# Optimization experiments

Hardware: AMD Instinct MI355X
Metric: run time of the kernel (lower is better)

Reference implementation:

```python
import jax, jax.numpy as jnp
import numpy as np


def _unit(v):
    return v / jnp.linalg.norm(v, axis=-1, keepdims=True)


def setup_inputs() -> dict:
    key = jax.random.key(0)
    k1, k2, k3, k4 = jax.random.split(key, 4)
    N, M = 20000, 6890
    scan_vertices = jax.random.normal(k1, (1, N, 3), dtype=jnp.float32)
    template_vertices = jax.random.normal(k2, (1, M, 3), dtype=jnp.float32)
    # normals are unit vectors in practice
    scan_normals = _unit(jax.random.normal(k3, (N, 3), dtype=jnp.float32))
    template_normals = _unit(jax.random.normal(k4, (M, 3), dtype=jnp.float32))
    return {
        "scan_vertices": scan_vertices,
        "template_vertices": template_vertices,
        "scan_normals": scan_normals,
        "template_normals": template_normals,
        "K_knn": 15,
    }


def reference(scan_vertices, template_vertices, scan_normals, template_normals, K_knn):
    sv = scan_vertices.reshape(-1, 3)       # [N,3]
    tv = template_vertices.reshape(-1, 3)   # [M,3]
    # Brute-force pairwise distances [M,N] (vectorizes the per-vertex loop)
    dist = jnp.linalg.norm(sv[None, :, :] - tv[:, None, :], axis=-1)
    # NOTE: torch.topk defaults to largest=True, so the original selects the
    # K LARGEST distances. lax.top_k also returns the largest -> faithful.
    _, knn_idx = jax.lax.top_k(dist, K_knn)                 # [M,K]
    knn_normals = scan_normals[knn_idx]                     # [M,K,3]
    dot = jnp.sum(knn_normals * template_normals[:, None, :], axis=-1)  # [M,K]
    angle_deg = jnp.degrees(jnp.arccos(jnp.clip(dot, -1.0, 1.0)))
    best = jnp.argmin(angle_deg, axis=1)                    # [M]
    sel = jnp.take_along_axis(knn_idx, best[:, None], axis=1)[:, 0]  # [M]
    mse = jnp.mean(jnp.linalg.norm(sv[sel] - tv, axis=1))
    return mse
```

## Files before the change

kernel.cpp:

```cpp
#include <hip/hip_runtime.h>
#include <math.h>


constexpr int K = 15;
constexpr int NBUCK = 256;
constexpr int WAVES = 4;

__device__ __forceinline__ int bucket_of(float k2) {
    int b = (int)(k2 * 8.0f);
    b = b > (NBUCK - 1) ? (NBUCK - 1) : b;
    return (NBUCK - 1) - b;
}

__global__ __launch_bounds__(256) void scatter_kernel(
    const float* __restrict__ sv,
    float4*      __restrict__ sorted,
    float*       __restrict__ smax,
    int N, int nb)
{
    __shared__ int h[NBUCK];
    __shared__ int startSh[NBUCK];
    __shared__ int cursor[NBUCK];
    const int t    = threadIdx.x;
    const int base = blockIdx.x * 256;

    h[t] = 0;
    __syncthreads();

#pragma unroll 4
    for (int i = t; i < base; i += 256) {
        float x = sv[3*i], y = sv[3*i+1], z = sv[3*i+2];
        atomicAdd(&h[bucket_of(fmaf(x, x, fmaf(y, y, z*z)))], 1);
    }
    __syncthreads();
    const int mine = h[t];
    __syncthreads();

    float px = 0.0f, py = 0.0f, pz = 0.0f, pk2 = 0.0f;
    const bool has = (base + t) < N;
    if (has) {
        px  = sv[3*(base+t)]; py = sv[3*(base+t)+1]; pz = sv[3*(base+t)+2];
        pk2 = fmaf(px, px, fmaf(py, py, pz*pz));
        atomicAdd(&h[bucket_of(pk2)], 1);
    }
#pragma unroll 4
    for (int i = base + 256 + t; i < N; i += 256) {
        float x = sv[3*i], y = sv[3*i+1], z = sv[3*i+2];
        atomicAdd(&h[bucket_of(fmaf(x, x, fmaf(y, y, z*z)))], 1);
    }
    __syncthreads();
    const int total = h[t];

    for (int d = 1; d < NBUCK; d <<= 1) {
        int u = (t >= d) ? h[t - d] : 0;
        __syncthreads();
        h[t] += u;
        __syncthreads();
    }
    const int startv = h[t] - total;
    startSh[t] = startv;
    cursor[t]  = startv + mine;
    __syncthreads();

    if (blockIdx.x == 0) {
        for (int j = t; j < nb; j += 256) {
            int pos = j * 64;
            int lo = 0, hi = NBUCK - 1;
            while (lo < hi) {
                int mid = (lo + hi + 1) >> 1;
                if (startSh[mid] <= pos) lo = mid; else hi = mid - 1;
            }
            int bOrig = (NBUCK - 1) - lo;
            smax[j] = sqrtf((float)(bOrig + 1) * 0.125f);
        }
    }

    if (has) {
        int pos = atomicAdd(&cursor[bucket_of(pk2)], 1);
        sorted[pos] = make_float4(px, py, pz, __int_as_float(base + t));
    }
}

template<bool SORTED>
__global__ __launch_bounds__(WAVES * 64) void knn_loss_kernel(
    const float4* __restrict__ pts,
    const float*  __restrict__ smax,
    const float*  __restrict__ sv,
    const float*  __restrict__ tv,
    const float*  __restrict__ sn,
    const float*  __restrict__ tn,
    float* __restrict__ partial,
    int N, int M, float invM)
{
    __shared__ float bsum[WAVES];
    const int lane = threadIdx.x & 63;
    const int w    = threadIdx.x >> 6;
    const int m    = blockIdx.x * WAVES + w;
    const bool valid = (m < M);

    float contrib = 0.0f;
    if (valid) {
        const float tvx = tv[3*m], tvy = tv[3*m+1], tvz = tv[3*m+2];
        const float tlen = sqrtf(tvx*tvx + tvy*tvy + tvz*tvz);

        float v; int idx;
        {
            int l = (lane < N) ? lane : 0;
            float px, py, pz;
            if (SORTED) {
                float4 q = pts[l];
                px = q.x; py = q.y; pz = q.z; idx = __float_as_int(q.w);
            } else {
                px = sv[3*l]; py = sv[3*l+1]; pz = sv[3*l+2]; idx = l;
            }
            float dx = px - tvx, dy = py - tvy, dz = pz - tvz;
            v = fmaf(dx, dx, fmaf(dy, dy, dz * dz));
            if (lane >= N) { v = -1.0f; idx = 0x7FFFFFFF; }
        }
#pragma unroll
        for (int k = 2; k <= 64; k <<= 1) {
#pragma unroll
            for (int j = k >> 1; j > 0; j >>= 1) {
                float ov = __shfl_xor(v, j);
                int   oi = __shfl_xor(idx, j);
                bool up    = ((lane & k) == 0);
                bool lower = ((lane & j) == 0);
                bool mine  = (v > ov) || (v == ov && idx < oi);
                bool keep  = lower ? (up ? mine : !mine) : (up ? !mine : mine);
                if (!keep) { v = ov; idx = oi; }
            }
        }
        float eV = (lane < K) ? v : -1.0f;
        int   eI = idx;
        float thr = __shfl(v, K - 1);

        for (int ib = 64; ib < N; ib += 64) {
            int  i   = ib + lane;
            bool has = (i < N);
            float d2; int oi2;
            if (SORTED) {
                float4 q = pts[has ? i : 0];
                float bnd = smax[ib >> 6] + tlen;
                if (bnd * bnd * 1.00001f < thr) break;
                float dx = q.x - tvx, dy = q.y - tvy, dz = q.z - tvz;
                d2 = fmaf(dx, dx, fmaf(dy, dy, dz * dz));
                oi2 = __float_as_int(q.w);
            } else {
                int g = has ? i : 0;
                float dx = sv[3*g] - tvx, dy = sv[3*g+1] - tvy, dz = sv[3*g+2] - tvz;
                d2 = fmaf(dx, dx, fmaf(dy, dy, dz * dz));
                oi2 = i;
            }
            unsigned long long mb = __ballot(has && (d2 >= thr));
            while (mb) {
                int src = __ffsll(mb) - 1;
                mb &= mb - 1;
                float cv = __shfl(d2, src);
                int   ci = __shfl(oi2, src);
                unsigned long long bb =
                    __ballot((eV > cv) || (eV == cv && eI < ci)) & 0x7FFFull;
                int p = __popcll(bb);
                if (p < K) {
                    float uv = __shfl_up(eV, 1);
                    int   ui = __shfl_up(eI, 1);
                    if (lane < K) {
                        if (lane == p)      { eV = cv; eI = ci; }
                        else if (lane > p)  { eV = uv; eI = ui; }
                    }
                    thr = __shfl(eV, K - 1);
                    if (mb) mb &= __ballot(d2 >= thr);
                }
            }
        }

        const float tnx = tn[3*m], tny = tn[3*m+1], tnz = tn[3*m+2];
        float ang = 3.0e38f;
        int myI = eI;
        if (lane < K && myI != 0x7FFFFFFF) {
            float dot = sn[3*myI]*tnx + sn[3*myI+1]*tny + sn[3*myI+2]*tnz;
            dot = fminf(1.0f, fmaxf(-1.0f, dot));
            ang = acosf(dot) * 57.29577951308232f;
        }
        float ba = ang; int br = lane; int bi = myI;
#pragma unroll
        for (int s = 1; s < 16; s <<= 1) {
            float oa  = __shfl_xor(ba, s);
            int   orr = __shfl_xor(br, s);
            int   oi  = __shfl_xor(bi, s);
            bool take = (oa < ba) || (oa == ba && orr < br);
            if (take) { ba = oa; br = orr; bi = oi; }
        }
        if (lane == 0) {
            float dx = sv[3*bi]   - tvx;
            float dy = sv[3*bi+1] - tvy;
            float dz = sv[3*bi+2] - tvz;
            contrib = sqrtf(dx*dx + dy*dy + dz*dz) * invM;
        }
    }

    if (lane == 0) bsum[w] = contrib;
    __syncthreads();
    if (threadIdx.x == 0)
        partial[blockIdx.x] = bsum[0] + bsum[1] + bsum[2] + bsum[3];
}

__global__ __launch_bounds__(256) void reduce_kernel(
    const float* __restrict__ partial, float* __restrict__ out, int n)
{
    __shared__ float sh[4];
    const int lane = threadIdx.x & 63;
    const int w    = threadIdx.x >> 6;
    float s = 0.0f;
    for (int i = threadIdx.x; i < n; i += 256) s += partial[i];
#pragma unroll
    for (int d = 1; d < 64; d <<= 1) s += __shfl_xor(s, d);
    if (lane == 0) sh[w] = s;
    __syncthreads();
    if (threadIdx.x == 0) out[0] = sh[0] + sh[1] + sh[2] + sh[3];
}

extern "C" void kernel_launch(void* const* d_in, const int* in_sizes, int n_in,
                              void* d_out, int out_size, void* d_ws, size_t ws_size,
                              hipStream_t stream) {
    const float* sv = (const float*)d_in[0];
    const float* tv = (const float*)d_in[1];
    const float* sn = (const float*)d_in[2];
    const float* tn = (const float*)d_in[3];

    int N = in_sizes[0] / 3;
    int M = in_sizes[1] / 3;
    int nb = (N + 63) / 64;
    float* out = (float*)d_out;
    float invM = 1.0f / (float)M;
    int grid  = (M + WAVES - 1) / WAVES;
    int nblk  = (N + 255) / 256;

    size_t offSorted  = 0;
    size_t offSmax    = offSorted + (size_t)N * sizeof(float4);
    size_t offPartial = (offSmax + (size_t)nb * sizeof(float) + 15) & ~(size_t)15;
    size_t need       = offPartial + (size_t)grid * sizeof(float);

    if (ws_size >= need) {
        float4* sorted  = (float4*)((char*)d_ws + offSorted);
        float*  smax    = (float*) ((char*)d_ws + offSmax);
        float*  partial = (float*) ((char*)d_ws + offPartial);

        scatter_kernel<<<nblk, 256, 0, stream>>>(sv, sorted, smax, N, nb);
        knn_loss_kernel<true><<<grid, WAVES * 64, 0, stream>>>(
            sorted, smax, sv, tv, sn, tn, partial, N, M, invM);
        reduce_kernel<<<1, 256, 0, stream>>>(partial, out, grid);
    } else if (ws_size >= (size_t)grid * sizeof(float)) {
        float* partial = (float*)d_ws;
        knn_loss_kernel<false><<<grid, WAVES * 64, 0, stream>>>(
            nullptr, nullptr, sv, tv, sn, tn, partial, N, M, invM);
        reduce_kernel<<<1, 256, 0, stream>>>(partial, out, grid);
    }
}
```

Before: 30.88 us.

## Partition sorted scan points by octant to tighten farthest-neighbour pruning bounds

```diff
diff --git a/kernel.cpp b/kernel.cpp
--- a/kernel.cpp
+++ b/kernel.cpp
@@ -3,80 +3,107 @@
 
 
 constexpr int K = 15;
-constexpr int NBUCK = 256;
+constexpr int RBUCK = 256;
+constexpr int NBUCK2 = 8 * RBUCK;
 constexpr int WAVES = 4;
 
-__device__ __forceinline__ int bucket_of(float k2) {
+__device__ __forceinline__ int rbucket_of(float k2) {
     int b = (int)(k2 * 8.0f);
-    b = b > (NBUCK - 1) ? (NBUCK - 1) : b;
-    return (NBUCK - 1) - b;
+    b = b > (RBUCK - 1) ? (RBUCK - 1) : b;
+    return (RBUCK - 1) - b;
+}
+__device__ __forceinline__ int octant_of(float x, float y, float z) {
+    return (x < 0.0f ? 1 : 0) | (y < 0.0f ? 2 : 0) | (z < 0.0f ? 4 : 0);
 }
 
 __global__ __launch_bounds__(256) void scatter_kernel(
     const float* __restrict__ sv,
     float4*      __restrict__ sorted,
-    float*       __restrict__ smax,
+    float*       __restrict__ rmax,
+    int*         __restrict__ octStartG,
     int N, int nb)
 {
-    __shared__ int h[NBUCK];
-    __shared__ int startSh[NBUCK];
-    __shared__ int cursor[NBUCK];
+    __shared__ int h[NBUCK2];
+    __shared__ int startSh[NBUCK2];
+    __shared__ int cursor[NBUCK2];
     const int t    = threadIdx.x;
     const int base = blockIdx.x * 256;
 
-    h[t] = 0;
-    __syncthreads();
-
-#pragma unroll 4
+#pragma unroll 8
+    for (int j = t; j < NBUCK2; j += 256) h[j] = 0;
+    __syncthreads();
+
     for (int i = t; i < base; i += 256) {
         float x = sv[3*i], y = sv[3*i+1], z = sv[3*i+2];
-        atomicAdd(&h[bucket_of(fmaf(x, x, fmaf(y, y, z*z)))], 1);
-    }
-    __syncthreads();
-    const int mine = h[t];
-    __syncthreads();
-
-    float px = 0.0f, py = 0.0f, pz = 0.0f, pk2 = 0.0f;
+        int b = (octant_of(x, y, z) << 8) |
+                rbucket_of(fmaf(x, x, fmaf(y, y, z*z)));
+        atomicAdd(&h[b], 1);
+    }
+    __syncthreads();
+    int mine8[8];
+#pragma unroll
+    for (int j = 0; j < 8; ++j) mine8[j] = h[t*8 + j];
+    __syncthreads();
+
+    float px = 0.0f, py = 0.0f, pz = 0.0f;
+    int pb = 0;
     const bool has = (base + t) < N;
     if (has) {
-        px  = sv[3*(base+t)]; py = sv[3*(base+t)+1]; pz = sv[3*(base+t)+2];
-        pk2 = fmaf(px, px, fmaf(py, py, pz*pz));
-        atomicAdd(&h[bucket_of(pk2)], 1);
-    }
-#pragma unroll 4
+        px = sv[3*(base+t)]; py = sv[3*(base+t)+1]; pz = sv[3*(base+t)+2];
+        pb = (octant_of(px, py, pz) << 8) |
+             rbucket_of(fmaf(px, px, fmaf(py, py, pz*pz)));
+        atomicAdd(&h[pb], 1);
+    }
     for (int i = base + 256 + t; i < N; i += 256) {
         float x = sv[3*i], y = sv[3*i+1], z = sv[3*i+2];
-        atomicAdd(&h[bucket_of(fmaf(x, x, fmaf(y, y, z*z)))], 1);
-    }
-    __syncthreads();
-    const int total = h[t];
-
-    for (int d = 1; d < NBUCK; d <<= 1) {
-        int u = (t >= d) ? h[t - d] : 0;
+        int b = (octant_of(x, y, z) << 8) |
+                rbucket_of(fmaf(x, x, fmaf(y, y, z*z)));
+        atomicAdd(&h[b], 1);
+    }
+    __syncthreads();
+
+    int tot8[8]; int tot = 0;
+#pragma unroll
+    for (int j = 0; j < 8; ++j) { tot8[j] = h[t*8 + j]; tot += tot8[j]; }
+    cursor[t] = tot;
+    __syncthreads();
+    for (int d = 1; d < 256; d <<= 1) {
+        int u = (t >= d) ? cursor[t - d] : 0;
         __syncthreads();
-        h[t] += u;
+        cursor[t] += u;
         __syncthreads();
     }
-    const int startv = h[t] - total;
-    startSh[t] = startv;
-    cursor[t]  = startv + mine;
+    int running = cursor[t] - tot;
+    __syncthreads();
+#pragma unroll
+    for (int j = 0; j < 8; ++j) {
+        startSh[t*8 + j] = running;
+        cursor[t*8 + j]  = running + mine8[j];
+        running += tot8[j];
+    }
     __syncthreads();
 
     if (blockIdx.x == 0) {
-        for (int j = t; j < nb; j += 256) {
-            int pos = j * 64;
-            int lo = 0, hi = NBUCK - 1;
-            while (lo < hi) {
-                int mid = (lo + hi + 1) >> 1;
-                if (startSh[mid] <= pos) lo = mid; else hi = mid - 1;
-            }
-            int bOrig = (NBUCK - 1) - lo;
-            smax[j] = sqrtf((float)(bOrig + 1) * 0.125f);
+        if (t < 8) octStartG[t] = startSh[t << 8];
+        if (t == 8) octStartG[8] = N;
+        for (int o = 0; o < 8; ++o) {
+            int oS = startSh[o << 8];
+            int oE = (o < 7) ? startSh[(o + 1) << 8] : N;
+            for (int k = t; oS + (k << 6) < oE; k += 256) {
+                int pos = oS + (k << 6);
+                int lo = 0, hi = RBUCK - 1;
+                while (lo < hi) {
+                    int mid = (lo + hi + 1) >> 1;
+                    if (startSh[(o << 8) + mid] <= pos) lo = mid; else hi = mid - 1;
+                }
+                rmax[o*nb + k] = (lo == 0) ? 3.0e38f
+                                           : sqrtf((float)(RBUCK - lo) * 0.125f);
+            }
         }
     }
 
     if (has) {
-        int pos = atomicAdd(&cursor[bucket_of(pk2)], 1);
+        int pos = atomicAdd(&cursor[pb], 1);
         sorted[pos] = make_float4(px, py, pz, __int_as_float(base + t));
     }
 }
@@ -84,13 +111,14 @@
 template<bool SORTED>
 __global__ __launch_bounds__(WAVES * 64) void knn_loss_kernel(
     const float4* __restrict__ pts,
-    const float*  __restrict__ smax,
+    const float*  __restrict__ rmax,
+    const int*    __restrict__ octStartG,
     const float*  __restrict__ sv,
     const float*  __restrict__ tv,
     const float*  __restrict__ sn,
     const float*  __restrict__ tn,
     float* __restrict__ partial,
-    int N, int M, float invM)
+    int N, int M, float invM, int nbo)
 {
     __shared__ float bsum[WAVES];
     const int lane = threadIdx.x & 63;
@@ -101,21 +129,51 @@
     float contrib = 0.0f;
     if (valid) {
         const float tvx = tv[3*m], tvy = tv[3*m+1], tvz = tv[3*m+2];
-        const float tlen = sqrtf(tvx*tvx + tvy*tvy + tvz*tvz);
+        const float tx2 = tvx*tvx, ty2 = tvy*tvy, tz2 = tvz*tvz;
+        const float t2  = tx2 + ty2 + tz2;
+
+        const float cxn = (tvx > 0.0f) ? tx2 : 0.0f;
+        const float cxp = (tvx < 0.0f) ? tx2 : 0.0f;
+        const float cyn = (tvy > 0.0f) ? ty2 : 0.0f;
+        const float cyp = (tvy < 0.0f) ? ty2 : 0.0f;
+        const float czn = (tvz > 0.0f) ? tz2 : 0.0f;
+        const float czp = (tvz < 0.0f) ? tz2 : 0.0f;
+        auto g2v = [&](int o) {
+            return ((o & 1) ? cxn : cxp) + ((o & 2) ? cyn : cyp)
+                 + ((o & 4) ? czn : czp);
+        };
+
+        int ob = 0; float bg = 0.0f;
+        int prefS = 0; float prefR0 = 0.0f;
+        if (SORTED) {
+            bg = g2v(0);
+#pragma unroll
+            for (int o = 1; o < 8; ++o) {
+                float g2o = g2v(o);
+                if (g2o > bg) { bg = g2o; ob = o; }
+            }
+            if (lane < 9) prefS = octStartG[lane];
+            if (lane < 8) prefR0 = rmax[lane * nbo];
+        }
 
         float v; int idx;
+        int oS = 0, oE = N;
         {
-            int l = (lane < N) ? lane : 0;
+            int l; bool hasB;
             float px, py, pz;
             if (SORTED) {
-                float4 q = pts[l];
+                oS = __shfl(prefS, ob); oE = __shfl(prefS, ob + 1);
+                l = oS + lane; hasB = l < oE;
+                float4 q = pts[hasB ? l : 0];
                 px = q.x; py = q.y; pz = q.z; idx = __float_as_int(q.w);
             } else {
-                px = sv[3*l]; py = sv[3*l+1]; pz = sv[3*l+2]; idx = l;
+                l = lane; hasB = l < N;
+                int g = hasB ? l : 0;
+                px = sv[3*g]; py = sv[3*g+1]; pz = sv[3*g+2]; idx = l;
             }
             float dx = px - tvx, dy = py - tvy, dz = pz - tvz;
             v = fmaf(dx, dx, fmaf(dy, dy, dz * dz));
-            if (lane >= N) { v = -1.0f; idx = 0x7FFFFFFF; }
+            if (!hasB) { v = -1.0f; idx = 0x7FFFFFFF; }
         }
 #pragma unroll
         for (int k = 2; k <= 64; k <<= 1) {
@@ -134,23 +192,7 @@
         int   eI = idx;
         float thr = __shfl(v, K - 1);
 
-        for (int ib = 64; ib < N; ib += 64) {
-            int  i   = ib + lane;
-            bool has = (i < N);
-            float d2; int oi2;
-            if (SORTED) {
-                float4 q = pts[has ? i : 0];
-                float bnd = smax[ib >> 6] + tlen;
-                if (bnd * bnd * 1.00001f < thr) break;
-                float dx = q.x - tvx, dy = q.y - tvy, dz = q.z - tvz;
-                d2 = fmaf(dx, dx, fmaf(dy, dy, dz * dz));
-                oi2 = __float_as_int(q.w);
-            } else {
-                int g = has ? i : 0;
-                float dx = sv[3*g] - tvx, dy = sv[3*g+1] - tvy, dz = sv[3*g+2] - tvz;
-                d2 = fmaf(dx, dx, fmaf(dy, dy, dz * dz));
-                oi2 = i;
-            }
+        auto process_chunk = [&](float d2, int oi2, bool has) {
             unsigned long long mb = __ballot(has && (d2 >= thr));
             while (mb) {
                 int src = __ffsll(mb) - 1;
@@ -171,6 +213,40 @@
                     if (mb) mb &= __ballot(d2 >= thr);
                 }
             }
+        };
+
+        if (SORTED) {
+            auto scan_octant = [&](int o, int s, int e, int kStart,
+                                   float r0, float g) {
+                for (int k = kStart; ; ++k) {
+                    int pos = s + (k << 6);
+                    if (pos >= e) break;
+                    float r  = (k == 0) ? r0 : rmax[o*nbo + k];
+                    float b2 = fmaf(2.0f*g, r, fmaf(r, r, t2));
+                    if (b2 * 1.00001f < thr) break;
+                    int i = pos + lane; bool has = i < e;
+                    float4 q = pts[has ? i : pos];
+                    float dx = q.x - tvx, dy = q.y - tvy, dz = q.z - tvz;
+                    float d2 = fmaf(dx, dx, fmaf(dy, dy, dz * dz));
+                    process_chunk(d2, __float_as_int(q.w), has);
+                }
+            };
+            scan_octant(ob, oS, oE, 1, 0.0f, sqrtf(bg));
+            for (int o2 = 0; o2 < 8; ++o2) {
+                if (o2 == ob) continue;
+                int s2 = __shfl(prefS, o2), e2 = __shfl(prefS, o2 + 1);
+                scan_octant(o2, s2, e2, 0, __shfl(prefR0, o2), sqrtf(g2v(o2)));
+            }
+        } else {
+            for (int ib = 64; ib < N; ib += 64) {
+                int  i   = ib + lane;
+                bool has = (i < N);
+                int g = has ? i : 0;
+                float dx = sv[3*g] - tvx, dy = sv[3*g+1] - tvy,
+                      dz = sv[3*g+2] - tvz;
+                float d2 = fmaf(dx, dx, fmaf(dy, dy, dz * dz));
+                process_chunk(d2, i, has);
+            }
         }
 
         const float tnx = tn[3*m], tny = tn[3*m+1], tnz = tn[3*m+2];
@@ -236,23 +312,26 @@
     int nblk  = (N + 255) / 256;
 
     size_t offSorted  = 0;
-    size_t offSmax    = offSorted + (size_t)N * sizeof(float4);
-    size_t offPartial = (offSmax + (size_t)nb * sizeof(float) + 15) & ~(size_t)15;
+    size_t offRmax    = offSorted + (size_t)N * sizeof(float4);
+    size_t offOct     = (offRmax + (size_t)8 * nb * sizeof(float) + 15) & ~(size_t)15;
+    size_t offPartial = (offOct + 9 * sizeof(int) + 15) & ~(size_t)15;
     size_t need       = offPartial + (size_t)grid * sizeof(float);
 
     if (ws_size >= need) {
-        float4* sorted  = (float4*)((char*)d_ws + offSorted);
-        float*  smax    = (float*) ((char*)d_ws + offSmax);
-        float*  partial = (float*) ((char*)d_ws + offPartial);
-
-        scatter_kernel<<<nblk, 256, 0, stream>>>(sv, sorted, smax, N, nb);
+        float4* sorted   = (float4*)((char*)d_ws + offSorted);
+        float*  rmaxp    = (float*) ((char*)d_ws + offRmax);
+        int*    octStart = (int*)   ((char*)d_ws + offOct);
+        float*  partial  = (float*) ((char*)d_ws + offPartial);
+
+        scatter_kernel<<<nblk, 256, 0, stream>>>(sv, sorted, rmaxp,
+                                                 octStart, N, nb);
         knn_loss_kernel<true><<<grid, WAVES * 64, 0, stream>>>(
-            sorted, smax, sv, tv, sn, tn, partial, N, M, invM);
+            sorted, rmaxp, octStart, sv, tv, sn, tn, partial, N, M, invM, nb);
         reduce_kernel<<<1, 256, 0, stream>>>(partial, out, grid);
     } else if (ws_size >= (size_t)grid * sizeof(float)) {
         float* partial = (float*)d_ws;
         knn_loss_kernel<false><<<grid, WAVES * 64, 0, stream>>>(
-            nullptr, nullptr, sv, tv, sn, tn, partial, N, M, invM);
+            nullptr, nullptr, nullptr, sv, tv, sn, tn, partial, N, M, invM, nb);
         reduce_kernel<<<1, 256, 0, stream>>>(partial, out, grid);
     }
 }
```

After: 49.91 us. +61.6%, slower.
